# Kernel tuning notes

Measured on AMD Instinct MI355X. Metric: run time of the kernel, lower is better.

Reference implementation:

```python
import jax, jax.numpy as jnp
import numpy as np

EPS = 1e-15
N, DIM, H, DH = 16384, 1024, 16, 64

# ---- stereographic (k<0, hyperbolic) math, per geoopt ----

def _sabs(k):
    return jnp.clip(jnp.abs(k), EPS, None)

def _tan_k(x, k):  # k < 0 branch of geoopt tan_k
    sk = jnp.sqrt(_sabs(k))
    return jnp.tanh(x * sk) / sk

def _artan_k(x, k):  # k < 0 branch of geoopt artan_k
    sk = jnp.sqrt(_sabs(k))
    return jnp.arctanh(jnp.clip(x * sk, -1.0 + 1e-7, 1.0 - 1e-7)) / sk

def _norm(x):
    return jnp.clip(jnp.sqrt(jnp.sum(x * x, -1, keepdims=True)), EPS, None)

def _project(x, k):
    n = _norm(x)
    maxnorm = (1.0 - 1e-5) / jnp.sqrt(_sabs(k))
    return jnp.where(n > maxnorm, x / n * maxnorm, x)

def _expmap0(u, k):
    un = _norm(u)
    return _tan_k(un, k) * u / un

def _logmap0(y, k):
    yn = _norm(y)
    return _artan_k(yn, k) * y / yn

def _mobius_add(x, y, k):
    x2 = jnp.sum(x * x, -1, keepdims=True)
    y2 = jnp.sum(y * y, -1, keepdims=True)
    xy = jnp.sum(x * y, -1, keepdims=True)
    num = (1 - 2 * k * xy - k * y2) * x + (1 + k * x2) * y
    den = jnp.clip(1 - 2 * k * xy + k * k * x2 * y2, EPS, None)
    return num / den

def _mobius_scalar_mul(r, x, k):
    xn = _norm(x)
    return _tan_k(r * _artan_k(xn, k), k) * x / xn

def _clamp_abs(x, eps):
    s = jnp.where(x >= 0, 1.0, -1.0)
    return s * jnp.clip(jnp.abs(x), eps, None)

# ---- StereographicLinear: mobius_matvec + mobius bias add, per head ----

def _stereo_linear(x, W, b, c, heads):
    n, fin = x.shape
    fout = W.shape[0]
    kk = c[None, :, None]  # per-head curvature
    u = _logmap0(x.reshape(n, heads, fin // heads), kk).reshape(n, fin)
    mu = (u @ W.T).reshape(n, heads, fout // heads)
    res = _project(_expmap0(mu, kk), kk)
    sb = _project(_expmap0(b.reshape(1, heads, fout // heads), kk), kk)
    res = _project(_mobius_add(res, sb, kk), kk)
    return res.reshape(n, fout)

# ---- GeometricLinearizedAttention ----

def _linear_attn(Q, K, V, mask, c):
    # Q, K, V: [H, n, d]; mask: [n]; c: [H]
    k = c[:, None, None]
    pt = jnp.clip(1.0 + k * jnp.sum(V * V, -1, keepdims=True), EPS, None)
    v1 = Q / pt                      # parallel_transport0back(V, Q)
    v2 = K / pt                      # parallel_transport0back(V, K)
    gamma = jnp.clip(2.0 / pt, EPS, None)  # lambda_x(V)
    den = _clamp_abs(gamma - 1.0, 1e-10)
    m = mask[None, :, None]
    x = gamma / den * V * m
    v1 = jax.nn.elu(v1) + 1.0
    v2 = den * (jax.nn.elu(v2) + 1.0) * m
    v2_sum = jnp.sum(v2, axis=-2)                    # [H, d]
    Dn = jnp.einsum('hnd,hd->hn', v1, v2_sum)
    D_inv = 1.0 / jnp.where(Dn == 0, 1e-5, Dn)
    ctx = jnp.einsum('hnd,hne->hde', v2, x)          # [H, d, d]
    Xo = jnp.einsum('hde,hnd,hn->hne', ctx, v1, D_inv)
    Xo = _project(Xo, k)
    Xo = _mobius_scalar_mul(0.5, Xo, k)
    return _project(Xo, k)


def setup_inputs() -> dict:
    key = jax.random.key(0)
    ks = jax.random.split(key, 11)
    hd = H * DH
    X = jax.random.normal(ks[0], (N, DIM), jnp.float32) * 0.05  # small norms -> inside Poincare ball
    mask = (jax.random.uniform(ks[1], (N,)) > 0.1).astype(jnp.float32)
    def lin(kk, fo, fi):
        return jax.random.normal(kk, (fo, fi), jnp.float32) / np.sqrt(fi).astype(np.float32)
    Wq = lin(ks[2], hd, DIM); bq = jnp.zeros((hd,), jnp.float32)
    Wk = lin(ks[3], hd, DIM); bk = jnp.zeros((hd,), jnp.float32)
    Wv = lin(ks[4], hd, DIM); bv = jax.random.normal(ks[5], (hd,), jnp.float32) * 0.01
    Wff = lin(ks[6], DIM, hd); bff = jax.random.normal(ks[7], (DIM,), jnp.float32) * 0.01
    c_v = -(jax.random.uniform(ks[8], (H,), jnp.float32) * 0.9 + 0.1)
    c_attn = -(jax.random.uniform(ks[9], (H,), jnp.float32) * 0.9 + 0.1)
    c_ff = -(jax.random.uniform(ks[10], (H,), jnp.float32) * 0.9 + 0.1)
    return dict(X=X, mask=mask, Wq=Wq, bq=bq, Wk=Wk, bk=bk, Wv=Wv, bv=bv,
                c_v=c_v, c_attn=c_attn, Wff=Wff, bff=bff, c_ff=c_ff)


def reference(X, mask, Wq, bq, Wk, bk, Wv, bv, c_v, c_attn, Wff, bff, c_ff):
    n = X.shape[0]
    def split(t):  # [n, H*DH] -> [H, n, DH]
        return t.reshape(n, H, DH).transpose(1, 0, 2)
    Q = split(X @ Wq.T + bq)
    K = split(X @ Wk.T + bk)
    V = split(_stereo_linear(X, Wv, bv, c_v, H))
    A = _linear_attn(Q, K, V, mask, c_attn)          # [H, n, DH]
    A = A.transpose(1, 0, 2).reshape(n, H * DH)
    return _stereo_linear(A, Wff, bff, c_ff, H)
```

## Files before the change

kernel.cpp:

```cpp
#include <hip/hip_runtime.h>
#include <math.h>
#include <stdint.h>

#define NTOK 16384
#define DIMF 1024
#define NH 16
#define DHD 64
#define NQK 2048

typedef _Float16 half_t;
typedef __attribute__((ext_vector_type(8))) _Float16 half8;
typedef __attribute__((ext_vector_type(4))) _Float16 half4;
typedef __attribute__((ext_vector_type(4))) float floatx4;

__device__ __forceinline__ float wsum(float v) {
  v += __shfl_xor(v, 32, 64);
  v += __shfl_xor(v, 16, 64);
  v += __shfl_xor(v, 8, 64);
  v += __shfl_xor(v, 4, 64);
  v += __shfl_xor(v, 2, 64);
  v += __shfl_xor(v, 1, 64);
  return v;
}

template <int CTRL>
__device__ __forceinline__ float dpp_add(float v) {
  int t = __builtin_amdgcn_update_dpp(0, __float_as_int(v), CTRL, 0xF, 0xF, true);
  return v + __int_as_float(t);
}
__device__ __forceinline__ float wsum16(float v) {
  v = dpp_add<0xB1>(v);
  v = dpp_add<0x4E>(v);
  v = dpp_add<0x124>(v);
  v = dpp_add<0x128>(v);
  return v;
}

__device__ __forceinline__ float frcp(float x) { return __builtin_amdgcn_rcpf(x); }
__device__ __forceinline__ float fexp(float x) { return __expf(x); }
__device__ __forceinline__ float flog(float x) { return __logf(x); }
__device__ __forceinline__ float ftanh_pos(float x) {
  float e = fexp(2.f * x);
  return 1.f - 2.f * frcp(e + 1.f);
}
__device__ __forceinline__ float fatanh01(float t) {
  return 0.5f * flog((1.f + t) * frcp(1.f - t));
}

__device__ __forceinline__ void gload16(const void* g, void* lds) {
  __builtin_amdgcn_global_load_lds(
      (const __attribute__((address_space(1))) uint32_t*)(uintptr_t)g,
      (__attribute__((address_space(3))) uint32_t*)(uintptr_t)lds, 16, 0, 0);
}

struct EpiArgs {
  const float* sb;
  const float* y2;
  const float* c_st;
  const float* c_at;
  const float* mask;
  half_t* Qh;
  half_t* Kh;
  half_t* v2T;
  half_t* xT;
  float* v2sum;
  int qstride;
};

template <int MODE, typename OutT>
__global__ __launch_bounds__(512, 2) void gemm_f16(const half_t* __restrict__ A,
                                                   const half_t* __restrict__ B,
                                                   const float* __restrict__ bias,
                                                   OutT* __restrict__ C,
                                                   int M, int Nn, int K, EpiArgs ep) {
  __shared__ half_t sA[2][256 * 64];
  __shared__ half_t sB[2][256 * 64];
  const int tid = threadIdx.x;
  const int lane = tid & 63;
  const int w = tid >> 6;
  const int wm = w >> 2;
  const int wn = w & 3;

  int gx = gridDim.x;
  int nwg = gx * gridDim.y;
  int lin = blockIdx.y * gx + blockIdx.x;
  int bx = blockIdx.x, by = blockIdx.y;
  if ((nwg & 7) == 0) {
    int cpx = nwg >> 3;
    int swz = (lin & 7) * cpx + (lin >> 3);
    bx = swz % gx;
    by = swz / gx;
  }
  const int n0 = bx * 256;
  const int m0 = by * 256;

  const half_t* pA[2];
  const half_t* pB[2];
#pragma unroll
  for (int t = 0; t < 2; ++t) {
    int g = 2 * w + t;
    pA[t] = A + (size_t)(m0 + g * 16 + (lane & 15)) * K + ((lane >> 4) << 3);
    pB[t] = B + (size_t)(n0 + g * 16 + (lane & 15)) * K + ((lane >> 4) << 3);
  }

  auto stageA = [&](int KS, int T, half_t* buf) {
#pragma unroll
    for (int t = 0; t < 2; ++t)
      gload16(pA[t] + KS * 32 + T * 64, buf + (KS * 16 + 2 * w + t) * 512);
  };
  auto stageB = [&](int KS, int T, half_t* buf) {
#pragma unroll
    for (int t = 0; t < 2; ++t)
      gload16(pB[t] + KS * 32 + T * 64, buf + (KS * 16 + 2 * w + t) * 512);
  };

  floatx4 acc[8][4];
#pragma unroll
  for (int i = 0; i < 8; ++i)
#pragma unroll
    for (int j = 0; j < 4; ++j) acc[i][j] = (floatx4){0.f, 0.f, 0.f, 0.f};

  const int NTt = K >> 6;

  stageA(0, 0, &sA[0][0]);
  stageB(0, 0, &sB[0][0]);
  stageA(1, 0, &sA[0][0]);
  stageB(1, 0, &sB[0][0]);
  stageA(0, 1, &sA[1][0]);
  stageB(0, 1, &sB[1][0]);
  asm volatile("s_waitcnt vmcnt(4)" ::: "memory");
  __builtin_amdgcn_s_barrier();

  for (int kt = 0; kt < NTt; ++kt) {
    const int c = kt & 1;
    half_t* sAc = c ? &sA[1][0] : &sA[0][0];
    half_t* sBc = c ? &sB[1][0] : &sB[0][0];
    half_t* sAn = c ? &sA[0][0] : &sA[1][0];
    half_t* sBn = c ? &sB[0][0] : &sB[1][0];

    {
      half8 b[4], a[8];
#pragma unroll
      for (int j = 0; j < 4; ++j)
        b[j] = *(const half8*)&sBc[(wn * 4 + j) * 512 + lane * 8];
#pragma unroll
      for (int i = 0; i < 8; ++i)
        a[i] = *(const half8*)&sAc[(wm * 8 + i) * 512 + lane * 8];
      if (kt + 1 < NTt) {
        stageA(1, kt + 1, sAn);
        stageB(1, kt + 1, sBn);
      }
      __builtin_amdgcn_s_barrier();
      __builtin_amdgcn_s_setprio(1);
#pragma unroll
      for (int i = 0; i < 8; ++i)
#pragma unroll
        for (int j = 0; j < 4; ++j)
          acc[i][j] = __builtin_amdgcn_mfma_f32_16x16x32_f16(a[i], b[j], acc[i][j], 0, 0, 0);
      __builtin_amdgcn_s_setprio(0);
      __builtin_amdgcn_s_barrier();
    }

    {
      half8 b[4], a[8];
#pragma unroll
      for (int j = 0; j < 4; ++j)
        b[j] = *(const half8*)&sBc[(16 + wn * 4 + j) * 512 + lane * 8];
#pragma unroll
      for (int i = 0; i < 8; ++i)
        a[i] = *(const half8*)&sAc[(16 + wm * 8 + i) * 512 + lane * 8];
      if (kt + 2 < NTt) {
        stageA(0, kt + 2, sAc);
        stageB(0, kt + 2, sBc);
      }
      __builtin_amdgcn_s_barrier();
      __builtin_amdgcn_s_setprio(1);
#pragma unroll
      for (int i = 0; i < 8; ++i)
#pragma unroll
        for (int j = 0; j < 4; ++j)
          acc[i][j] = __builtin_amdgcn_mfma_f32_16x16x32_f16(a[i], b[j], acc[i][j], 0, 0, 0);
      __builtin_amdgcn_s_setprio(0);
      if (kt < NTt - 2)
        asm volatile("s_waitcnt vmcnt(4)" ::: "memory");
      else
        asm volatile("s_waitcnt vmcnt(0)" ::: "memory");
      __builtin_amdgcn_s_barrier();
    }
  }

  const int e = lane & 15;
  const int quad = lane >> 4;

  if constexpr (MODE == 0) {
#pragma unroll
    for (int j = 0; j < 4; ++j) {
      int col = n0 + wn * 64 + j * 16 + e;
      float bv = bias ? bias[col] : 0.f;
#pragma unroll
      for (int i = 0; i < 8; ++i) {
        int row = m0 + wm * 128 + i * 16 + quad * 4;
#pragma unroll
        for (int r = 0; r < 4; ++r)
          C[(size_t)(row + r) * Nn + col] = (OutT)(acc[i][j][r] + bv);
      }
    }
  } else {
    const int hb = n0 + wn * 64;
    const int h = hb >> 6;
    const float kst = ep.c_st[h];
    const float sk = sqrtf(fmaxf(fabsf(kst), 1e-15f));
    const float rsk = frcp(sk);
    const float maxn = (1.f - 1e-5f) * rsk;
    const float mx2 = maxn * maxn;
    float sbj[4];
#pragma unroll
    for (int j = 0; j < 4; ++j) sbj[j] = ep.sb[hb + j * 16 + e];
    const float y2h = ep.y2[h];
    float ka = 0.f, v2acc[4] = {0.f, 0.f, 0.f, 0.f};
    if constexpr (MODE == 1) ka = ep.c_at[h];
    const int rowbase = m0 + wm * 128;

#pragma unroll
    for (int i = 0; i < 8; ++i) {
      half4 v2s[4], xs[4];
#pragma unroll
      for (int r = 0; r < 4; ++r) {
        const int row = rowbase + i * 16 + quad * 4 + r;
        float qraw[4], kraw[4];
        float mrow = 0.f;
        size_t qb = 0;
        if constexpr (MODE == 1) {
          qb = (size_t)row * ep.qstride + hb + e;
#pragma unroll
          for (int j = 0; j < 4; ++j) {
            qraw[j] = (float)ep.Qh[qb + j * 16];
            kraw[j] = (float)ep.Kh[qb + j * 16];
          }
          mrow = ep.mask[row];
        }
        float s = 0.f, dp = 0.f;
#pragma unroll
        for (int j = 0; j < 4; ++j) {
          float mv = acc[i][j][r];
          s += mv * mv;
          dp += mv * sbj[j];
        }
        s = wsum16(s);
        dp = wsum16(dp);
        float un = fmaxf(sqrtf(s), 1e-15f);
        float tn = ftanh_pos(un * sk) * rsk;
        float f = tn * frcp(un);
        float rn = fmaxf(tn, 1e-15f);
        if (rn > maxn) { f *= maxn * frcp(rn); rn = maxn; }
        float xy = dp * f;
        float x2 = rn * rn;
        float num1 = 1.f - 2.f * kst * xy - kst * y2h;
        float num2 = 1.f + kst * x2;
        float den = fmaxf(1.f - 2.f * kst * xy + kst * kst * x2 * y2h, 1e-15f);
        float rden = frcp(den);
        float c1 = num1 * f * rden;
        float c2 = num2 * rden;
        float o[4];
        float os = 0.f;
#pragma unroll
        for (int j = 0; j < 4; ++j) {
          o[j] = c1 * acc[i][j][r] + c2 * sbj[j];
          os += o[j] * o[j];
        }
        os = wsum16(os);
        float on = fmaxf(sqrtf(os), 1e-15f);
        if (on > maxn) {
          float sc = maxn * frcp(on);
#pragma unroll
          for (int j = 0; j < 4; ++j) o[j] *= sc;
        }
        if constexpr (MODE == 2) {
#pragma unroll
          for (int j = 0; j < 4; ++j)
            C[(size_t)row * Nn + hb + j * 16 + e] = (OutT)o[j];
        } else {
          float vn2 = fminf(os, mx2);
          float pt = fmaxf(1.f + ka * vn2, 1e-15f);
          float rpt = frcp(pt);
          float gamma = fmaxf(2.f * rpt, 1e-15f);
          float gm1 = gamma - 1.f;
          float aden = fmaxf(fabsf(gm1), 1e-10f);
          float den2 = (gm1 >= 0.f) ? aden : -aden;
          float xsc = gamma * frcp(den2) * mrow;
#pragma unroll
          for (int j = 0; j < 4; ++j) {
            float q = qraw[j] * rpt;
            float v1 = (q > 0.f) ? (q + 1.f) : fexp(q);
            ep.Qh[qb + j * 16] = (half_t)v1;
            float kv = kraw[j] * rpt;
            float v2 = den2 * ((kv > 0.f) ? (kv + 1.f) : fexp(kv)) * mrow;
            v2acc[j] += v2;
            v2s[j][r] = (half_t)v2;
            xs[j][r] = (half_t)(xsc * o[j]);
          }
        }
      }
      if constexpr (MODE == 1) {
        const size_t tb0 = (size_t)(rowbase + i * 16 + quad * 4);
#pragma unroll
        for (int j = 0; j < 4; ++j) {
          size_t tb = (size_t)(hb + j * 16 + e) * NTOK + tb0;
          *(half4*)&ep.v2T[tb] = v2s[j];
          *(half4*)&ep.xT[tb] = xs[j];
        }
      }
    }
    if constexpr (MODE == 1) {
#pragma unroll
      for (int j = 0; j < 4; ++j) {
        float t = v2acc[j];
        t += __shfl_xor(t, 16, 64);
        t += __shfl_xor(t, 32, 64);
        if (quad == 0) atomicAdd(&ep.v2sum[h * DHD + j * 16 + e], t);
      }
    }
  }
}

struct WPack {
  const float* w[4];
  half_t* h[4];
};
__global__ __launch_bounds__(256) void convert_w_kernel(WPack pk) {
  int wi = blockIdx.y;
  const float* w = pk.w[wi];
  half_t* ph = pk.h[wi];
  int i = (blockIdx.x * 256 + threadIdx.x) * 4;
  float4 v = *(const float4*)&w[i];
  half4 hh = {(half_t)v.x, (half_t)v.y, (half_t)v.z, (half_t)v.w};
  *(half4*)&ph[i] = hh;
}

__global__ __launch_bounds__(128) void prep_sb_kernel(const float* __restrict__ bv,
                                                      const float* __restrict__ cv,
                                                      const float* __restrict__ bf,
                                                      const float* __restrict__ cf,
                                                      const float* __restrict__ bq,
                                                      const float* __restrict__ bk,
                                                      float* __restrict__ sbV,
                                                      float* __restrict__ y2V,
                                                      float* __restrict__ sbF,
                                                      float* __restrict__ y2F,
                                                      float* __restrict__ bqk) {
  int tid = threadIdx.x;
  for (int i = tid; i < 1024; i += 128) {
    bqk[i] = bq[i];
    bqk[1024 + i] = bk[i];
  }
  int wv = tid >> 6;
  int lane = tid & 63;
  const float* b = wv ? bf : bv;
  const float* c = wv ? cf : cv;
  float* sb = wv ? sbF : sbV;
  float* y2 = wv ? y2F : y2V;
  for (int h = 0; h < NH; ++h) {
    float k = c[h];
    float sk = sqrtf(fmaxf(fabsf(k), 1e-15f));
    float rsk = frcp(sk);
    float maxn = (1.f - 1e-5f) * rsk;
    float bb = b[h * DHD + lane];
    float bs = wsum(bb * bb);
    float bn = fmaxf(sqrtf(bs), 1e-15f);
    float tb = ftanh_pos(bn * sk) * rsk;
    float sv = tb * frcp(bn) * bb;
    float sbn = fmaxf(tb, 1e-15f);
    if (sbn > maxn) { sv *= maxn * frcp(sbn); sbn = maxn; }
    sb[h * DHD + lane] = sv;
    if (lane == 0) y2[h] = sbn * sbn;
  }
}

__global__ __launch_bounds__(256) void prep_kernel(const float* __restrict__ X,
                                                   half_t* __restrict__ Xh,
                                                   half_t* __restrict__ U,
                                                   const float* __restrict__ c) {
  int lane = threadIdx.x & 63;
  int wid = blockIdx.x * 4 + (threadIdx.x >> 6);
  int nw = gridDim.x * 4;
  int sub = lane >> 4;
  for (int row = wid; row < NTOK; row += nw) {
#pragma unroll
    for (int ch = 0; ch < 4; ++ch) {
      int h = ch * 4 + sub;
      int idx = row * DIMF + ch * 256 + lane * 4;
      float4 x = *(const float4*)&X[idx];
      float s = x.x * x.x + x.y * x.y + x.z * x.z + x.w * x.w;
      s = wsum16(s);
      float k = c[h];
      float sk = sqrtf(fmaxf(fabsf(k), 1e-15f));
      float yn = fmaxf(sqrtf(s), 1e-15f);
      float t = fminf(yn * sk, 1.f - 1e-7f);
      float f = fatanh01(t) * frcp(sk) * frcp(yn);
      half4 xh4 = {(half_t)x.x, (half_t)x.y, (half_t)x.z, (half_t)x.w};
      *(half4*)&Xh[idx] = xh4;
      half4 u4 = {(half_t)(x.x * f), (half_t)(x.y * f), (half_t)(x.z * f), (half_t)(x.w * f)};
      *(half4*)&U[idx] = u4;
    }
  }
}

__global__ __launch_bounds__(256) void attn_pass2(const half_t* __restrict__ v2T,
                                                  const half_t* __restrict__ xT,
                                                  float* __restrict__ ctxT) {
  __shared__ float red[4096];
  int tid = threadIdx.x;
  int h = blockIdx.y;
  for (int i = tid; i < 4096; i += 256) red[i] = 0.f;
  __syncthreads();
  int lane = tid & 63;
  int w = tid >> 6;
  int m = lane & 15;
  int q = lane >> 4;
  const half_t* xb = xT + (size_t)h * 64 * NTOK;
  const half_t* vb = v2T + (size_t)h * 64 * NTOK;
  floatx4 acc[4][4];
#pragma unroll
  for (int i = 0; i < 4; ++i)
#pragma unroll
    for (int j = 0; j < 4; ++j) acc[i][j] = (floatx4){0.f, 0.f, 0.f, 0.f};

  int tok0 = blockIdx.x * 512 + w * 32 + q * 8;
#pragma unroll
  for (int c = 0; c < 4; ++c) {
    int tk = tok0 + c * 128;
    half8 af[4], bf[4];
#pragma unroll
    for (int i = 0; i < 4; ++i)
      af[i] = *(const half8*)&xb[(size_t)(i * 16 + m) * NTOK + tk];
#pragma unroll
    for (int j = 0; j < 4; ++j)
      bf[j] = *(const half8*)&vb[(size_t)(j * 16 + m) * NTOK + tk];
#pragma unroll
    for (int i = 0; i < 4; ++i)
#pragma unroll
      for (int j = 0; j < 4; ++j)
        acc[i][j] = __builtin_amdgcn_mfma_f32_16x16x32_f16(af[i], bf[j], acc[i][j], 0, 0, 0);
  }
#pragma unroll
  for (int i = 0; i < 4; ++i)
#pragma unroll
    for (int j = 0; j < 4; ++j)
#pragma unroll
      for (int r = 0; r < 4; ++r) {
        int e = i * 16 + q * 4 + r;
        int d = j * 16 + m;
        atomicAdd(&red[e * 64 + d], acc[i][j][r]);
      }
  __syncthreads();
  float* dst = ctxT + (size_t)h * 4096;
  for (int i = tid; i < 4096; i += 256) atomicAdd(&dst[i], red[i]);
}

__global__ __launch_bounds__(256) void attn_pass3m(const half_t* __restrict__ v1h,
                                                   const float* __restrict__ ctxT,
                                                   const float* __restrict__ v2sum,
                                                   const float* __restrict__ c_at,
                                                   const float* __restrict__ c_ff,
                                                   half_t* __restrict__ Uff,
                                                   int sv1) {
  __shared__ half_t sctx[8 * 64 * 8];
  int tid = threadIdx.x;
  int h = blockIdx.y;
  int m0 = blockIdx.x * 64;
  for (int ci = tid; ci < 512; ci += 256) {
    int t = ci >> 6, l = ci & 63;
    int j = t & 3, ks = t >> 2;
    int e2 = j * 16 + (l & 15);
    int d = ks * 32 + (l >> 4) * 8;
    const float* src = &ctxT[h * 4096 + e2 * 64 + d];
    half8 hh;
#pragma unroll
    for (int q = 0; q < 8; ++q) hh[q] = (half_t)src[q];
    *(half8*)&sctx[ci * 8] = hh;
  }
  __syncthreads();

  int lane = tid & 63;
  int w = tid >> 6;
  int quad = lane >> 4;
  int e = lane & 15;

  const half_t* ap = v1h + (size_t)(m0 + w * 16 + e) * sv1 + h * DHD + quad * 8;
  half8 a0 = *(const half8*)ap;
  half8 a1 = *(const half8*)(ap + 32);

  const float* vsp = v2sum + h * DHD + quad * 8;
  float4 va = *(const float4*)&vsp[0];
  float4 vb = *(const float4*)&vsp[4];
  float4 vc = *(const float4*)&vsp[32];
  float4 vd = *(const float4*)&vsp[36];
  float dn = (float)a0[0] * va.x + (float)a0[1] * va.y + (float)a0[2] * va.z + (float)a0[3] * va.w +
             (float)a0[4] * vb.x + (float)a0[5] * vb.y + (float)a0[6] * vb.z + (float)a0[7] * vb.w +
             (float)a1[0] * vc.x + (float)a1[1] * vc.y + (float)a1[2] * vc.z + (float)a1[3] * vc.w +
             (float)a1[4] * vd.x + (float)a1[5] * vd.y + (float)a1[6] * vd.z + (float)a1[7] * vd.w;
  dn += __shfl_xor(dn, 16, 64);
  dn += __shfl_xor(dn, 32, 64);
  float di = frcp((dn == 0.f) ? 1e-5f : dn);

  floatx4 acc[4];
#pragma unroll
  for (int j = 0; j < 4; ++j) acc[j] = (floatx4){0.f, 0.f, 0.f, 0.f};
#pragma unroll
  for (int j = 0; j < 4; ++j) {
    half8 b0 = *(const half8*)&sctx[((0 * 4 + j) * 64 + lane) * 8];
    half8 b1 = *(const half8*)&sctx[((1 * 4 + j) * 64 + lane) * 8];
    acc[j] = __builtin_amdgcn_mfma_f32_16x16x32_f16(a0, b0, acc[j], 0, 0, 0);
    acc[j] = __builtin_amdgcn_mfma_f32_16x16x32_f16(a1, b1, acc[j], 0, 0, 0);
  }

  float ka = c_at[h];
  float sk_a = sqrtf(fmaxf(fabsf(ka), 1e-15f));
  float rsk_a = frcp(sk_a);
  float maxn_a = (1.f - 1e-5f) * rsk_a;
  float kf = c_ff[h];
  float sk_f = sqrtf(fmaxf(fabsf(kf), 1e-15f));
  float rsk_f = frcp(sk_f);

#pragma unroll
  for (int r = 0; r < 4; ++r) {
    float Di = __shfl(di, quad * 4 + r, 64);
    float v0 = acc[0][r], v1 = acc[1][r], v2 = acc[2][r], v3 = acc[3][r];
    float s = v0 * v0 + v1 * v1 + v2 * v2 + v3 * v3;
    s = wsum16(s);
    int row = m0 + w * 16 + quad * 4 + r;
    float f = Di;
    float xn = fmaxf(sqrtf(s) * Di, 1e-15f);
    if (xn > maxn_a) { f *= maxn_a * frcp(xn); xn = maxn_a; }
    float t = fminf(xn * sk_a, 1.f - 1e-7f);
    float ar = fatanh01(t) * rsk_a;
    float tk = ftanh_pos(0.5f * ar * sk_a) * rsk_a;
    f *= tk * frcp(xn);
    float nn = tk;
    if (nn > maxn_a) { f *= maxn_a * frcp(nn); nn = maxn_a; }
    float fn = fmaxf(nn, 1e-15f);
    float t2 = fminf(fn * sk_f, 1.f - 1e-7f);
    float ar2 = fatanh01(t2) * rsk_f;
    f *= ar2 * frcp(fn);
    size_t base = (size_t)row * DIMF + h * DHD + e;
    Uff[base + 0] = (half_t)(v0 * f);
    Uff[base + 16] = (half_t)(v1 * f);
    Uff[base + 32] = (half_t)(v2 * f);
    Uff[base + 48] = (half_t)(v3 * f);
  }
}

extern "C" void kernel_launch(void* const* d_in, const int* in_sizes, int n_in,
                              void* d_out, int out_size, void* d_ws, size_t ws_size,
                              hipStream_t stream) {
  const float* X = (const float*)d_in[0];
  const float* mask = (const float*)d_in[1];
  const float* Wq = (const float*)d_in[2];
  const float* bq = (const float*)d_in[3];
  const float* Wk = (const float*)d_in[4];
  const float* bk = (const float*)d_in[5];
  const float* Wv = (const float*)d_in[6];
  const float* bv = (const float*)d_in[7];
  const float* c_v = (const float*)d_in[8];
  const float* c_at = (const float*)d_in[9];
  const float* Wff = (const float*)d_in[10];
  const float* bff = (const float*)d_in[11];
  const float* c_ff = (const float*)d_in[12];
  float* out = (float*)d_out;

  const size_t NE = (size_t)NTOK * DIMF;
  float* v2sum = (float*)d_ws;
  float* ctxT = v2sum + 1024;
  float* sbV = ctxT + 65536;
  float* sbF = sbV + 1024;
  float* y2V = sbF + 1024;
  float* y2F = y2V + 16;
  float* bqk = y2F + 16;
  half_t* H1 = (half_t*)(bqk + 2048);
  half_t* H2 = H1 + NE;
  half_t* HQK = H2 + NE;
  half_t* V2T = HQK + 2 * NE;
  half_t* XT = V2T + NE;
  half_t* Wh0 = XT + NE;

  WPack pk;
  pk.w[0] = Wq; pk.w[1] = Wk; pk.w[2] = Wv; pk.w[3] = Wff;
  for (int i = 0; i < 4; ++i) pk.h[i] = Wh0 + (size_t)i * DIMF * DIMF;

  EpiArgs epN{};
  EpiArgs epV{sbV, y2V, c_v, c_at, mask, HQK, HQK + 1024, V2T, XT, v2sum, NQK};
  EpiArgs epF{sbF, y2F, c_ff, nullptr, nullptr, nullptr, nullptr, nullptr, nullptr, nullptr, 0};

  convert_w_kernel<<<dim3(1024, 4), 256, 0, stream>>>(pk);
  prep_sb_kernel<<<1, 128, 0, stream>>>(bv, c_v, bff, c_ff, bq, bk, sbV, y2V, sbF, y2F, bqk);
  prep_kernel<<<512, 256, 0, stream>>>(X, H1, H2, c_v);
  hipMemsetAsync(v2sum, 0, (1024 + 65536) * sizeof(float), stream);
  gemm_f16<0, half_t><<<dim3(NQK / 256, NTOK / 256), 512, 0, stream>>>(
      H1, pk.h[0], bqk, HQK, NTOK, NQK, DIMF, epN);
  gemm_f16<1, half_t><<<dim3(DIMF / 256, NTOK / 256), 512, 0, stream>>>(
      H2, pk.h[2], nullptr, (half_t*)nullptr, NTOK, DIMF, DIMF, epV);
  attn_pass2<<<dim3(NTOK / 512, NH), 256, 0, stream>>>(V2T, XT, ctxT);
  attn_pass3m<<<dim3(NTOK / 64, NH), 256, 0, stream>>>(HQK, ctxT, v2sum, c_at, c_ff, H1, NQK);
  gemm_f16<2, float><<<dim3(DIMF / 256, NTOK / 256), 512, 0, stream>>>(
      H1, pk.h[3], nullptr, out, NTOK, DIMF, DIMF, epF);
}
```

Measured before the change: 499.9 us.

## Halve GEMM K-tile to 32 and simplify double-buffered pipeline for higher occupancy

Shrinks the shared-memory A/B tiles from a 64-wide K slab to a 32-wide slab. This halves LDS use per block, and raises launch bounds to request 4 blocks per CU. The two-half, vmcnt-tuned prefetch schedule becomes a plain double-buffered loop that prefetches the next slab and ends each step with __syncthreads. The aim is more resident workgroups to hide latency. The risk: the 128-float accumulator per thread may not fit the tighter register budget, causing spills. The full sync per step also reduces overlap between loads and MFMA.

After: 1.787 ms. 3.57x slower.

```diff
diff --git a/kernel.cpp b/kernel.cpp
--- a/kernel.cpp
+++ b/kernel.cpp
@@ -68,13 +68,13 @@
 };
 
 template <int MODE, typename OutT>
-__global__ __launch_bounds__(512, 2) void gemm_f16(const half_t* __restrict__ A,
+__global__ __launch_bounds__(512, 4) void gemm_f16(const half_t* __restrict__ A,
                                                    const half_t* __restrict__ B,
                                                    const float* __restrict__ bias,
                                                    OutT* __restrict__ C,
                                                    int M, int Nn, int K, EpiArgs ep) {
-  __shared__ half_t sA[2][256 * 64];
-  __shared__ half_t sB[2][256 * 64];
+  __shared__ half_t sA[2][256 * 32];
+  __shared__ half_t sB[2][256 * 32];
   const int tid = threadIdx.x;
   const int lane = tid & 63;
   const int w = tid >> 6;
@@ -103,15 +103,15 @@
     pB[t] = B + (size_t)(n0 + g * 16 + (lane & 15)) * K + ((lane >> 4) << 3);
   }
 
-  auto stageA = [&](int KS, int T, half_t* buf) {
+  auto stageA = [&](int T, half_t* buf) {
 #pragma unroll
     for (int t = 0; t < 2; ++t)
-      gload16(pA[t] + KS * 32 + T * 64, buf + (KS * 16 + 2 * w + t) * 512);
+      gload16(pA[t] + T * 32, buf + (2 * w + t) * 512);
   };
-  auto stageB = [&](int KS, int T, half_t* buf) {
+  auto stageB = [&](int T, half_t* buf) {
 #pragma unroll
     for (int t = 0; t < 2; ++t)
-      gload16(pB[t] + KS * 32 + T * 64, buf + (KS * 16 + 2 * w + t) * 512);
+      gload16(pB[t] + T * 32, buf + (2 * w + t) * 512);
   };
 
   floatx4 acc[8][4];
@@ -120,73 +120,38 @@
 #pragma unroll
     for (int j = 0; j < 4; ++j) acc[i][j] = (floatx4){0.f, 0.f, 0.f, 0.f};
 
-  const int NTt = K >> 6;
-
-  stageA(0, 0, &sA[0][0]);
-  stageB(0, 0, &sB[0][0]);
-  stageA(1, 0, &sA[0][0]);
-  stageB(1, 0, &sB[0][0]);
-  stageA(0, 1, &sA[1][0]);
-  stageB(0, 1, &sB[1][0]);
-  asm volatile("s_waitcnt vmcnt(4)" ::: "memory");
-  __builtin_amdgcn_s_barrier();
-
-  for (int kt = 0; kt < NTt; ++kt) {
-    const int c = kt & 1;
+  const int NTt = K >> 5;
+
+  stageA(0, &sA[0][0]);
+  stageB(0, &sB[0][0]);
+  __syncthreads();
+
+  for (int s = 0; s < NTt; ++s) {
+    const int c = s & 1;
     half_t* sAc = c ? &sA[1][0] : &sA[0][0];
     half_t* sBc = c ? &sB[1][0] : &sB[0][0];
     half_t* sAn = c ? &sA[0][0] : &sA[1][0];
     half_t* sBn = c ? &sB[0][0] : &sB[1][0];
 
-    {
-      half8 b[4], a[8];
+    half8 b[4], a[8];
+#pragma unroll
+    for (int j = 0; j < 4; ++j)
+      b[j] = *(const half8*)&sBc[(wn * 4 + j) * 512 + lane * 8];
+#pragma unroll
+    for (int i = 0; i < 8; ++i)
+      a[i] = *(const half8*)&sAc[(wm * 8 + i) * 512 + lane * 8];
+    if (s + 1 < NTt) {
+      stageA(s + 1, sAn);
+      stageB(s + 1, sBn);
+    }
+    __builtin_amdgcn_s_setprio(1);
+#pragma unroll
+    for (int i = 0; i < 8; ++i)
 #pragma unroll
       for (int j = 0; j < 4; ++j)
-        b[j] = *(const half8*)&sBc[(wn * 4 + j) * 512 + lane * 8];
-#pragma unroll
-      for (int i = 0; i < 8; ++i)
-        a[i] = *(const half8*)&sAc[(wm * 8 + i) * 512 + lane * 8];
-      if (kt + 1 < NTt) {
-        stageA(1, kt + 1, sAn);
-        stageB(1, kt + 1, sBn);
-      }
-      __builtin_amdgcn_s_barrier();
-      __builtin_amdgcn_s_setprio(1);
-#pragma unroll
-      for (int i = 0; i < 8; ++i)
-#pragma unroll
-        for (int j = 0; j < 4; ++j)
-          acc[i][j] = __builtin_amdgcn_mfma_f32_16x16x32_f16(a[i], b[j], acc[i][j], 0, 0, 0);
-      __builtin_amdgcn_s_setprio(0);
-      __builtin_amdgcn_s_barrier();
-    }
-
-    {
-      half8 b[4], a[8];
-#pragma unroll
-      for (int j = 0; j < 4; ++j)
-        b[j] = *(const half8*)&sBc[(16 + wn * 4 + j) * 512 + lane * 8];
-#pragma unroll
-      for (int i = 0; i < 8; ++i)
-        a[i] = *(const half8*)&sAc[(16 + wm * 8 + i) * 512 + lane * 8];
-      if (kt + 2 < NTt) {
-        stageA(0, kt + 2, sAc);
-        stageB(0, kt + 2, sBc);
-      }
-      __builtin_amdgcn_s_barrier();
-      __builtin_amdgcn_s_setprio(1);
-#pragma unroll
-      for (int i = 0; i < 8; ++i)
-#pragma unroll
-        for (int j = 0; j < 4; ++j)
-          acc[i][j] = __builtin_amdgcn_mfma_f32_16x16x32_f16(a[i], b[j], acc[i][j], 0, 0, 0);
-      __builtin_amdgcn_s_setprio(0);
-      if (kt < NTt - 2)
-        asm volatile("s_waitcnt vmcnt(4)" ::: "memory");
-      else
-        asm volatile("s_waitcnt vmcnt(0)" ::: "memory");
-      __builtin_amdgcn_s_barrier();
-    }
+        acc[i][j] = __builtin_amdgcn_mfma_f32_16x16x32_f16(a[i], b[j], acc[i][j], 0, 0, 0);
+    __builtin_amdgcn_s_setprio(0);
+    __syncthreads();
   }
 
   const int e = lane & 15;
```
